# Kernel tuning notes

Hardware: AMD Instinct MI355X
Metric: run time of the kernel (lower is better)

## Reference

```python
import jax, jax.numpy as jnp
import numpy as np

N = 100_000          # ent_num
D = 256              # ent_dim
E_RAND = 3_200_000   # random edges (avg degree 32); + N self loops
NEG_SLOPE = 0.2      # LeakyReLU slope used by SpGraphAttentionLayer


def setup_inputs() -> dict:
    key = jax.random.key(0)
    k0, k1, k2, k3, k4, k5 = jax.random.split(key, 6)
    edges_rand = jax.random.randint(k0, (2, E_RAND), 0, N, dtype=jnp.int32)
    self_loops = jnp.tile(jnp.arange(N, dtype=jnp.int32)[None, :], (2, 1))
    edges = jnp.concatenate([edges_rand, self_loops], axis=1)  # [2, E]
    scale_w = 1.0 / np.sqrt(D).astype(np.float32)
    scale_a = 0.1 / np.sqrt(D).astype(np.float32)
    emb = jax.random.normal(k1, (N, D), jnp.float32)
    W1 = jax.random.normal(k2, (D, D), jnp.float32) * scale_w
    a1 = jax.random.normal(k3, (2 * D,), jnp.float32) * scale_a
    W2 = jax.random.normal(k4, (D, D), jnp.float32) * scale_w
    a2 = jax.random.normal(k5, (2 * D,), jnp.float32) * scale_a
    return {"emb": emb, "W1": W1, "a1": a1, "W2": W2, "a2": a2, "edges": edges}


def gat_layer(h, W, a, src, dst):
    # h: [N, D] node features; edges (src -> aggregates from dst)
    h2 = h @ W                              # [N, D]
    s_src = h2 @ a[:D]                      # [N] contribution of a . h_src
    s_dst = h2 @ a[D:]                      # [N] contribution of a . h_dst
    score = s_src[src] + s_dst[dst]         # [E] = a . [h_src; h_dst]
    e = jnp.exp(-jax.nn.leaky_relu(score, NEG_SLOPE))  # [E], pyGAT sparse form
    denom = jax.ops.segment_sum(e, src, num_segments=h.shape[0])          # [N]
    num = jax.ops.segment_sum(e[:, None] * h2[dst], src,
                              num_segments=h.shape[0])                    # [N, D]
    return jax.nn.elu(num / denom[:, None])


def reference(emb, W1, a1, W2, a2, edges):
    src, dst = edges[0], edges[1]
    h = gat_layer(emb, W1, a1, src, dst)
    h = gat_layer(h, W2, a2, src, dst)
    return h
```

## Files before the change

### kernel.cpp

```cpp
#include <hip/hip_runtime.h>
#include <hip/hip_bf16.h>

#define D 256
#define NEG_SLOPE 0.2f
#define BM 128
#define BN 128
#define BK 64
#define LDK 72

using bf16x8 = __attribute__((ext_vector_type(8))) __bf16;
using f32x4  = __attribute__((ext_vector_type(4))) float;
using u32x4  = __attribute__((ext_vector_type(4))) unsigned int;

__device__ __forceinline__ float bf2f(unsigned short u) {
    return __uint_as_float(((unsigned int)u) << 16);
}
__device__ __forceinline__ unsigned short f2bf(float f) {
    unsigned int u = __float_as_uint(f);
    unsigned int r = (u + 0x7FFF + ((u >> 16) & 1)) >> 16;
    return (unsigned short)r;
}


__global__ __launch_bounds__(256) void prep_kernel(
    const float* __restrict__ W1, const float* __restrict__ W2,
    unsigned short* __restrict__ WT1, unsigned short* __restrict__ WT2,
    int4* __restrict__ zbase, int nz16)
{
    const int b = blockIdx.x, tid = threadIdx.x;
    if (b < 256) {
        WT1[(size_t)tid * D + b] = f2bf(W1[(size_t)b * D + tid]);
    } else if (b < 512) {
        const int k = b - 256;
        WT2[(size_t)tid * D + k] = f2bf(W2[(size_t)k * D + tid]);
    } else {
        const int w = (b - 512) * 256 + tid;
        if (w < nz16) zbase[w] = make_int4(0, 0, 0, 0);
    }
}


__global__ void count_kernel(const int* __restrict__ src, int* __restrict__ counts, int E) {
    int t = blockIdx.x * blockDim.x + threadIdx.x;
    if (t < E) atomicAdd(&counts[src[t]], 1);
}

__global__ __launch_bounds__(1024) void scan_all_kernel(
    const int* __restrict__ counts, int* __restrict__ row_ptr, int n)
{
    __shared__ int ws[16];
    const int tid = threadIdx.x;
    const int lane = tid & 63, wv = tid >> 6;
    int base = 0;
    for (int c0 = 0; c0 < n; c0 += 4096) {
        const int idx = c0 + tid * 4;
        int4 v = make_int4(0, 0, 0, 0);
        if (idx + 3 < n) v = *(const int4*)(counts + idx);
        else {
            if (idx + 0 < n) v.x = counts[idx + 0];
            if (idx + 1 < n) v.y = counts[idx + 1];
            if (idx + 2 < n) v.z = counts[idx + 2];
            if (idx + 3 < n) v.w = counts[idx + 3];
        }
        const int s = v.x + v.y + v.z + v.w;
        int x = s;
        #pragma unroll
        for (int off = 1; off < 64; off <<= 1) {
            int t = __shfl_up(x, off);
            if (lane >= off) x += t;
        }
        if (lane == 63) ws[wv] = x;
        __syncthreads();
        int wo = base;
        #pragma unroll
        for (int w = 0; w < 16; ++w) if (w < wv) wo += ws[w];
        const int excl = wo + x - s;
        if (idx + 0 < n) row_ptr[idx + 0] = excl;
        if (idx + 1 < n) row_ptr[idx + 1] = excl + v.x;
        if (idx + 2 < n) row_ptr[idx + 2] = excl + v.x + v.y;
        if (idx + 3 < n) row_ptr[idx + 3] = excl + v.x + v.y + v.z;
        int tot = 0;
        #pragma unroll
        for (int w = 0; w < 16; ++w) tot += ws[w];
        __syncthreads();
        base += tot;
    }
    if (tid == 0) row_ptr[n] = base;
}

__global__ void fill_kernel(const int* __restrict__ src, const int* __restrict__ dst,
                            const int* __restrict__ row_ptr, int* __restrict__ fillp,
                            int* __restrict__ col, int E) {
    int t = blockIdx.x * blockDim.x + threadIdx.x;
    if (t < E) {
        int s = src[t];
        int pos = atomicAdd(&fillp[s], 1);
        col[row_ptr[s] + pos] = dst[t];
    }
}


__global__ __launch_bounds__(256) void gemm_mfma(
    const unsigned short* __restrict__ Ab, const float* __restrict__ Af,
    const unsigned short* __restrict__ BT,
    unsigned short* __restrict__ C, int M,
    const float* __restrict__ av, float* __restrict__ s_src, float* __restrict__ s_dst)
{
    __shared__ unsigned short smem[2 * BM * LDK];
    unsigned short* As_ = smem;
    unsigned short* Bs_ = smem + BM * LDK;
    const int tid = threadIdx.x;
    const int m0 = blockIdx.x * BM;
    const int n0 = blockIdx.y * BN;
    const int lane = tid & 63;
    const int wv = tid >> 6;
    const int wm = (wv & 1) * 64;
    const int wn = (wv >> 1) * 64;
    const int l15 = lane & 15;
    const int quad = lane >> 4;

    f32x4 acc[4][4];
    #pragma unroll
    for (int i = 0; i < 4; ++i)
        #pragma unroll
        for (int j = 0; j < 4; ++j)
            acc[i][j] = (f32x4){0.f, 0.f, 0.f, 0.f};

    for (int k0 = 0; k0 < D; k0 += BK) {
        #pragma unroll
        for (int c = tid; c < BM * 8; c += 256) {
            const int row = c >> 3, j = c & 7;
            const int gr = m0 + row;
            uint4 avv = make_uint4(0, 0, 0, 0);
            if (gr < M) {
                if (Af) {
                    const float* p = Af + (size_t)gr * D + k0 + j * 8;
                    const float4 f0 = *(const float4*)p;
                    const float4 f1 = *(const float4*)(p + 4);
                    avv.x = (unsigned int)f2bf(f0.x) | ((unsigned int)f2bf(f0.y) << 16);
                    avv.y = (unsigned int)f2bf(f0.z) | ((unsigned int)f2bf(f0.w) << 16);
                    avv.z = (unsigned int)f2bf(f1.x) | ((unsigned int)f2bf(f1.y) << 16);
                    avv.w = (unsigned int)f2bf(f1.z) | ((unsigned int)f2bf(f1.w) << 16);
                } else {
                    avv = *(const uint4*)(Ab + (size_t)gr * D + k0 + j * 8);
                }
            }
            *(uint4*)(As_ + row * LDK + j * 8) = avv;
            const uint4 bv = *(const uint4*)(BT + (size_t)(n0 + row) * D + k0 + j * 8);
            *(uint4*)(Bs_ + row * LDK + j * 8) = bv;
        }
        __syncthreads();
        #pragma unroll
        for (int s = 0; s < 2; ++s) {
            bf16x8 af[4], bfr[4];
            #pragma unroll
            for (int i = 0; i < 4; ++i)
                af[i] = *(const bf16x8*)(As_ + (wm + i * 16 + l15) * LDK + s * 32 + quad * 8);
            #pragma unroll
            for (int j = 0; j < 4; ++j)
                bfr[j] = *(const bf16x8*)(Bs_ + (wn + j * 16 + l15) * LDK + s * 32 + quad * 8);
            #pragma unroll
            for (int i = 0; i < 4; ++i)
                #pragma unroll
                for (int j = 0; j < 4; ++j)
                    acc[i][j] = __builtin_amdgcn_mfma_f32_16x16x32_bf16(
                        af[i], bfr[j], acc[i][j], 0, 0, 0);
        }
        __syncthreads();
    }

    unsigned short* Cw = smem + wv * (64 * LDK);
    #pragma unroll
    for (int i = 0; i < 4; ++i)
        #pragma unroll
        for (int j = 0; j < 4; ++j)
            #pragma unroll
            for (int r = 0; r < 4; ++r)
                Cw[(i * 16 + quad * 4 + r) * LDK + j * 16 + l15] = f2bf(acc[i][j][r]);
    __syncthreads();
    const int ccol = n0 + wn + (lane & 31) * 2;
    const float a1c0 = av[ccol],     a1c1 = av[ccol + 1];
    const float a2c0 = av[D + ccol], a2c1 = av[D + ccol + 1];
    #pragma unroll
    for (int rr = 0; rr < 64; rr += 2) {
        const int row = rr + (lane >> 5);
        const unsigned int wd = *(const unsigned int*)(Cw + row * LDK + (lane & 31) * 2);
        const int gr = m0 + wm + row;
        if (gr < M)
            *(unsigned int*)(C + (size_t)gr * D + ccol) = wd;
        const float f0 = bf2f((unsigned short)(wd & 0xffffu));
        const float f1 = bf2f((unsigned short)(wd >> 16));
        float p1 = f0 * a1c0 + f1 * a1c1;
        float p2 = f0 * a2c0 + f1 * a2c1;
        #pragma unroll
        for (int off = 16; off > 0; off >>= 1) {
            p1 += __shfl_xor(p1, off);
            p2 += __shfl_xor(p2, off);
        }
        if ((lane & 31) == 0 && gr < M) {
            atomicAdd(&s_src[gr], p1);
            atomicAdd(&s_dst[gr], p2);
        }
    }
}


__global__ __launch_bounds__(256) void agg_kernel(
    const unsigned short* __restrict__ h2, const float* __restrict__ s_src,
    const float* __restrict__ s_dst, const int* __restrict__ row_ptr,
    const int* __restrict__ col, unsigned short* __restrict__ out_bf16,
    float* __restrict__ out_f32, int Nn)
{
    const int lane = threadIdx.x & 63;
    const int half = lane >> 5;
    const int hl = lane & 31;
    const int node = blockIdx.x * 4 + (threadIdx.x >> 6);
    if (node >= Nn) return;
    const int beg = row_ptr[node], end = row_ptr[node + 1];
    const float ssrc = s_src[node];
    const unsigned short* hp = h2 + hl * 8;

    float a[8];
    #pragma unroll
    for (int i = 0; i < 8; ++i) a[i] = 0.f;
    float dpart = 0.f;

    for (int c0 = beg; c0 < end; c0 += 64) {
        const int cnt = min(64, end - c0);
        int j = 0;
        float e = 0.f;
        if (lane < cnt) {
            j = col[c0 + lane];
            const float sc = ssrc + s_dst[j];
            const float l = sc >= 0.f ? sc : NEG_SLOPE * sc;
            e = __expf(-l);
        }
        dpart += e;
        for (int k = 0; k < cnt; k += 8) {
            const int   j0 = __shfl(j, k + 0 + half);
            const int   j1 = __shfl(j, k + 2 + half);
            const int   j2 = __shfl(j, k + 4 + half);
            const int   j3 = __shfl(j, k + 6 + half);
            const float e0 = __shfl(e, k + 0 + half);
            const float e1 = __shfl(e, k + 2 + half);
            const float e2 = __shfl(e, k + 4 + half);
            const float e3 = __shfl(e, k + 6 + half);
            const uint4 u0 = *(const uint4*)(hp + (size_t)j0 * D);
            const uint4 u1 = *(const uint4*)(hp + (size_t)j1 * D);
            const uint4 u2 = *(const uint4*)(hp + (size_t)j2 * D);
            const uint4 u3 = *(const uint4*)(hp + (size_t)j3 * D);
            #define ACC8(u, ev)                                               \
                a[0] = fmaf(ev, __uint_as_float((u).x << 16), a[0]);          \
                a[1] = fmaf(ev, __uint_as_float((u).x & 0xffff0000u), a[1]);  \
                a[2] = fmaf(ev, __uint_as_float((u).y << 16), a[2]);          \
                a[3] = fmaf(ev, __uint_as_float((u).y & 0xffff0000u), a[3]);  \
                a[4] = fmaf(ev, __uint_as_float((u).z << 16), a[4]);          \
                a[5] = fmaf(ev, __uint_as_float((u).z & 0xffff0000u), a[5]);  \
                a[6] = fmaf(ev, __uint_as_float((u).w << 16), a[6]);          \
                a[7] = fmaf(ev, __uint_as_float((u).w & 0xffff0000u), a[7]);
            ACC8(u0, e0)
            ACC8(u1, e1)
            ACC8(u2, e2)
            ACC8(u3, e3)
            #undef ACC8
        }
    }

    #pragma unroll
    for (int i = 0; i < 8; ++i) a[i] += __shfl_xor(a[i], 32);

    float denom = dpart;
    #pragma unroll
    for (int off = 32; off > 0; off >>= 1) denom += __shfl_xor(denom, off);
    const float inv = 1.f / denom;

    if (half == 0) {
        float v[8];
        #pragma unroll
        for (int i = 0; i < 8; ++i) {
            const float x = a[i] * inv;
            v[i] = x > 0.f ? x : expm1f(x);
        }
        if (out_bf16) {
            u32x4 o;
            o.x = (unsigned int)f2bf(v[0]) | ((unsigned int)f2bf(v[1]) << 16);
            o.y = (unsigned int)f2bf(v[2]) | ((unsigned int)f2bf(v[3]) << 16);
            o.z = (unsigned int)f2bf(v[4]) | ((unsigned int)f2bf(v[5]) << 16);
            o.w = (unsigned int)f2bf(v[6]) | ((unsigned int)f2bf(v[7]) << 16);
            __builtin_nontemporal_store(o, (u32x4*)(out_bf16 + (size_t)node * D + hl * 8));
        } else {
            float* p = out_f32 + (size_t)node * D + hl * 8;
            f32x4 o0 = {v[0], v[1], v[2], v[3]};
            f32x4 o1 = {v[4], v[5], v[6], v[7]};
            __builtin_nontemporal_store(o0, (f32x4*)p);
            __builtin_nontemporal_store(o1, (f32x4*)(p + 4));
        }
    }
}


static inline size_t align_up(size_t x, size_t a) { return (x + a - 1) & ~(a - 1); }

extern "C" void kernel_launch(void* const* d_in, const int* in_sizes, int n_in,
                              void* d_out, int out_size, void* d_ws, size_t ws_size,
                              hipStream_t stream)
{
    const float* emb = (const float*)d_in[0];
    const float* W1  = (const float*)d_in[1];
    const float* a1  = (const float*)d_in[2];
    const float* W2  = (const float*)d_in[3];
    const float* a2  = (const float*)d_in[4];
    const int* edges = (const int*)d_in[5];
    const int Nn = in_sizes[0] / D;
    const int E  = in_sizes[5] / 2;
    const int* src = edges;
    const int* dst = edges + E;

    size_t off = 0;
    char* base = (char*)d_ws;
    unsigned short* hA = (unsigned short*)(base + off);
    off = align_up(off + (size_t)Nn * D * sizeof(unsigned short), 256);
    unsigned short* hB = (unsigned short*)(base + off);
    off = align_up(off + (size_t)Nn * D * sizeof(unsigned short), 256);
    unsigned short* WT1 = (unsigned short*)(base + off);
    off = align_up(off + (size_t)D * D * sizeof(unsigned short), 256);
    unsigned short* WT2 = (unsigned short*)(base + off);
    off = align_up(off + (size_t)D * D * sizeof(unsigned short), 256);

    const size_t cstride = align_up((size_t)Nn * sizeof(int), 256);
    char* zstart = base + off;
    float* s1s = (float*)(base + off); off += (size_t)Nn * sizeof(float);
    float* s1d = (float*)(base + off); off += (size_t)Nn * sizeof(float);
    float* s2s = (float*)(base + off); off += (size_t)Nn * sizeof(float);
    float* s2d = (float*)(base + off); off += (size_t)Nn * sizeof(float);
    off = align_up(off, 256);
    int* counts  = (int*)(base + off);   off += cstride;
    int* fillp   = (int*)(base + off);   off += cstride;
    const size_t zbytes = (size_t)(base + off - zstart);
    const int nz16 = (int)(zbytes / 16);

    int* row_ptr = (int*)(base + off);   off = align_up(off + (size_t)(Nn + 1) * sizeof(int), 256);
    int* col     = (int*)(base + off);   off = align_up(off + (size_t)E * sizeof(int), 256);

    const int zblocks = (nz16 + 255) / 256;
    prep_kernel<<<512 + zblocks, 256, 0, stream>>>(W1, W2, WT1, WT2, (int4*)zstart, nz16);

    count_kernel<<<(E + 255) / 256, 256, 0, stream>>>(src, counts, E);
    scan_all_kernel<<<1, 1024, 0, stream>>>(counts, row_ptr, Nn);
    fill_kernel<<<(E + 255) / 256, 256, 0, stream>>>(src, dst, row_ptr, fillp, col, E);

    dim3 ggrid((Nn + BM - 1) / BM, D / BN);
    gemm_mfma<<<ggrid, 256, 0, stream>>>(nullptr, emb, WT1, hA, Nn, a1, s1s, s1d);
    agg_kernel<<<(Nn + 3) / 4, 256, 0, stream>>>(hA, s1s, s1d, row_ptr, col, hB, nullptr, Nn);
    gemm_mfma<<<ggrid, 256, 0, stream>>>(hB, nullptr, WT2, hA, Nn, a2, s2s, s2d);
    agg_kernel<<<(Nn + 3) / 4, 256, 0, stream>>>(hA, s2s, s2d, row_ptr, col, nullptr,
                                                 (float*)d_out, Nn);
}
```

Measured before the change: 1.087 ms.

## Parallelize CSR prefix scan across blocks and use grid-stride count/fill/agg kernels

Replaces the single-block serial scan over all node counts with a three-phase scan: per-chunk sums, one small block scanning the chunk totals, then a parallel write of row offsets. The count, fill and aggregation kernels become grid-stride loops launched with a fixed 2048-block grid instead of one block per small work unit. The aim is to remove the long single-workgroup scan and reduce block launch overhead. It adds two extra small kernel launches, and the chunk scan assumes at most 128 chunks, so it only handles up to about 131K nodes.

```diff
diff --git a/kernel.cpp b/kernel.cpp
--- a/kernel.cpp
+++ b/kernel.cpp
@@ -7,6 +7,7 @@
 #define BN 128
 #define BK 64
 #define LDK 72
+#define SCAN_CHUNK 1024
 
 using bf16x8 = __attribute__((ext_vector_type(8))) __bf16;
 using f32x4  = __attribute__((ext_vector_type(4))) float;
@@ -41,58 +42,93 @@
 
 
 __global__ void count_kernel(const int* __restrict__ src, int* __restrict__ counts, int E) {
-    int t = blockIdx.x * blockDim.x + threadIdx.x;
-    if (t < E) atomicAdd(&counts[src[t]], 1);
-}
-
-__global__ __launch_bounds__(1024) void scan_all_kernel(
-    const int* __restrict__ counts, int* __restrict__ row_ptr, int n)
-{
-    __shared__ int ws[16];
+    const int stride = gridDim.x * blockDim.x;
+    for (int t = blockIdx.x * blockDim.x + threadIdx.x; t < E; t += stride)
+        atomicAdd(&counts[src[t]], 1);
+}
+
+__global__ __launch_bounds__(256) void scan_partial_kernel(
+    const int* __restrict__ counts, int* __restrict__ partial, int n)
+{
+    __shared__ int ws[4];
     const int tid = threadIdx.x;
     const int lane = tid & 63, wv = tid >> 6;
-    int base = 0;
-    for (int c0 = 0; c0 < n; c0 += 4096) {
-        const int idx = c0 + tid * 4;
-        int4 v = make_int4(0, 0, 0, 0);
-        if (idx + 3 < n) v = *(const int4*)(counts + idx);
-        else {
-            if (idx + 0 < n) v.x = counts[idx + 0];
-            if (idx + 1 < n) v.y = counts[idx + 1];
-            if (idx + 2 < n) v.z = counts[idx + 2];
-            if (idx + 3 < n) v.w = counts[idx + 3];
-        }
-        const int s = v.x + v.y + v.z + v.w;
-        int x = s;
-        #pragma unroll
-        for (int off = 1; off < 64; off <<= 1) {
-            int t = __shfl_up(x, off);
-            if (lane >= off) x += t;
-        }
-        if (lane == 63) ws[wv] = x;
+    const int idx = blockIdx.x * SCAN_CHUNK + tid * 4;
+    int4 v = make_int4(0, 0, 0, 0);
+    if (idx + 3 < n) v = *(const int4*)(counts + idx);
+    else {
+        if (idx + 0 < n) v.x = counts[idx + 0];
+        if (idx + 1 < n) v.y = counts[idx + 1];
+        if (idx + 2 < n) v.z = counts[idx + 2];
+        if (idx + 3 < n) v.w = counts[idx + 3];
+    }
+    int s = v.x + v.y + v.z + v.w;
+    #pragma unroll
+    for (int off = 32; off > 0; off >>= 1) s += __shfl_xor(s, off);
+    if (lane == 0) ws[wv] = s;
+    __syncthreads();
+    if (tid == 0) partial[blockIdx.x] = ws[0] + ws[1] + ws[2] + ws[3];
+}
+
+__global__ __launch_bounds__(128) void scan_chunks_kernel(
+    const int* __restrict__ partial, int* __restrict__ chunkoff,
+    int* __restrict__ row_ptr, int nchunks, int n)
+{
+    __shared__ int sm[128];
+    const int tid = threadIdx.x;
+    const int v = (tid < nchunks) ? partial[tid] : 0;
+    sm[tid] = v;
+    __syncthreads();
+    #pragma unroll
+    for (int off = 1; off < 128; off <<= 1) {
+        int t = (tid >= off) ? sm[tid - off] : 0;
         __syncthreads();
-        int wo = base;
-        #pragma unroll
-        for (int w = 0; w < 16; ++w) if (w < wv) wo += ws[w];
-        const int excl = wo + x - s;
-        if (idx + 0 < n) row_ptr[idx + 0] = excl;
-        if (idx + 1 < n) row_ptr[idx + 1] = excl + v.x;
-        if (idx + 2 < n) row_ptr[idx + 2] = excl + v.x + v.y;
-        if (idx + 3 < n) row_ptr[idx + 3] = excl + v.x + v.y + v.z;
-        int tot = 0;
-        #pragma unroll
-        for (int w = 0; w < 16; ++w) tot += ws[w];
+        sm[tid] += t;
         __syncthreads();
-        base += tot;
-    }
-    if (tid == 0) row_ptr[n] = base;
+    }
+    if (tid < nchunks) chunkoff[tid] = sm[tid] - v;
+    if (tid == 127) row_ptr[n] = sm[127];
+}
+
+__global__ __launch_bounds__(256) void scan_write_kernel(
+    const int* __restrict__ counts, const int* __restrict__ chunkoff,
+    int* __restrict__ row_ptr, int n)
+{
+    __shared__ int wsum[4];
+    const int tid = threadIdx.x;
+    const int lane = tid & 63, wv = tid >> 6;
+    const int idx = blockIdx.x * SCAN_CHUNK + tid * 4;
+    int4 v = make_int4(0, 0, 0, 0);
+    if (idx + 3 < n) v = *(const int4*)(counts + idx);
+    else {
+        if (idx + 0 < n) v.x = counts[idx + 0];
+        if (idx + 1 < n) v.y = counts[idx + 1];
+        if (idx + 2 < n) v.z = counts[idx + 2];
+        if (idx + 3 < n) v.w = counts[idx + 3];
+    }
+    const int s = v.x + v.y + v.z + v.w;
+    int x = s;
+    #pragma unroll
+    for (int off = 1; off < 64; off <<= 1) {
+        int t = __shfl_up(x, off);
+        if (lane >= off) x += t;
+    }
+    if (lane == 63) wsum[wv] = x;
+    __syncthreads();
+    int wo = chunkoff[blockIdx.x];
+    for (int w = 0; w < 4; ++w) if (w < wv) wo += wsum[w];
+    int excl = wo + x - s;
+    if (idx + 0 < n) row_ptr[idx + 0] = excl;
+    if (idx + 1 < n) row_ptr[idx + 1] = excl + v.x;
+    if (idx + 2 < n) row_ptr[idx + 2] = excl + v.x + v.y;
+    if (idx + 3 < n) row_ptr[idx + 3] = excl + v.x + v.y + v.z;
 }
 
 __global__ void fill_kernel(const int* __restrict__ src, const int* __restrict__ dst,
                             const int* __restrict__ row_ptr, int* __restrict__ fillp,
                             int* __restrict__ col, int E) {
-    int t = blockIdx.x * blockDim.x + threadIdx.x;
-    if (t < E) {
+    const int stride = gridDim.x * blockDim.x;
+    for (int t = blockIdx.x * blockDim.x + threadIdx.x; t < E; t += stride) {
         int s = src[t];
         int pos = atomicAdd(&fillp[s], 1);
         col[row_ptr[s] + pos] = dst[t];
@@ -214,86 +250,89 @@
     const int lane = threadIdx.x & 63;
     const int half = lane >> 5;
     const int hl = lane & 31;
-    const int node = blockIdx.x * 4 + (threadIdx.x >> 6);
-    if (node >= Nn) return;
-    const int beg = row_ptr[node], end = row_ptr[node + 1];
-    const float ssrc = s_src[node];
+    const int wid = blockIdx.x * 4 + (threadIdx.x >> 6);
+    const int nwaves = gridDim.x * 4;
     const unsigned short* hp = h2 + hl * 8;
 
-    float a[8];
-    #pragma unroll
-    for (int i = 0; i < 8; ++i) a[i] = 0.f;
-    float dpart = 0.f;
-
-    for (int c0 = beg; c0 < end; c0 += 64) {
-        const int cnt = min(64, end - c0);
-        int j = 0;
-        float e = 0.f;
-        if (lane < cnt) {
-            j = col[c0 + lane];
-            const float sc = ssrc + s_dst[j];
-            const float l = sc >= 0.f ? sc : NEG_SLOPE * sc;
-            e = __expf(-l);
-        }
-        dpart += e;
-        for (int k = 0; k < cnt; k += 8) {
-            const int   j0 = __shfl(j, k + 0 + half);
-            const int   j1 = __shfl(j, k + 2 + half);
-            const int   j2 = __shfl(j, k + 4 + half);
-            const int   j3 = __shfl(j, k + 6 + half);
-            const float e0 = __shfl(e, k + 0 + half);
-            const float e1 = __shfl(e, k + 2 + half);
-            const float e2 = __shfl(e, k + 4 + half);
-            const float e3 = __shfl(e, k + 6 + half);
-            const uint4 u0 = *(const uint4*)(hp + (size_t)j0 * D);
-            const uint4 u1 = *(const uint4*)(hp + (size_t)j1 * D);
-            const uint4 u2 = *(const uint4*)(hp + (size_t)j2 * D);
-            const uint4 u3 = *(const uint4*)(hp + (size_t)j3 * D);
-            #define ACC8(u, ev)                                               \
-                a[0] = fmaf(ev, __uint_as_float((u).x << 16), a[0]);          \
-                a[1] = fmaf(ev, __uint_as_float((u).x & 0xffff0000u), a[1]);  \
-                a[2] = fmaf(ev, __uint_as_float((u).y << 16), a[2]);          \
-                a[3] = fmaf(ev, __uint_as_float((u).y & 0xffff0000u), a[3]);  \
-                a[4] = fmaf(ev, __uint_as_float((u).z << 16), a[4]);          \
-                a[5] = fmaf(ev, __uint_as_float((u).z & 0xffff0000u), a[5]);  \
-                a[6] = fmaf(ev, __uint_as_float((u).w << 16), a[6]);          \
-                a[7] = fmaf(ev, __uint_as_float((u).w & 0xffff0000u), a[7]);
-            ACC8(u0, e0)
-            ACC8(u1, e1)
-            ACC8(u2, e2)
-            ACC8(u3, e3)
-            #undef ACC8
-        }
-    }
-
-    #pragma unroll
-    for (int i = 0; i < 8; ++i) a[i] += __shfl_xor(a[i], 32);
-
-    float denom = dpart;
-    #pragma unroll
-    for (int off = 32; off > 0; off >>= 1) denom += __shfl_xor(denom, off);
-    const float inv = 1.f / denom;
-
-    if (half == 0) {
-        float v[8];
-        #pragma unroll
-        for (int i = 0; i < 8; ++i) {
-            const float x = a[i] * inv;
-            v[i] = x > 0.f ? x : expm1f(x);
-        }
-        if (out_bf16) {
-            u32x4 o;
-            o.x = (unsigned int)f2bf(v[0]) | ((unsigned int)f2bf(v[1]) << 16);
-            o.y = (unsigned int)f2bf(v[2]) | ((unsigned int)f2bf(v[3]) << 16);
-            o.z = (unsigned int)f2bf(v[4]) | ((unsigned int)f2bf(v[5]) << 16);
-            o.w = (unsigned int)f2bf(v[6]) | ((unsigned int)f2bf(v[7]) << 16);
-            __builtin_nontemporal_store(o, (u32x4*)(out_bf16 + (size_t)node * D + hl * 8));
-        } else {
-            float* p = out_f32 + (size_t)node * D + hl * 8;
-            f32x4 o0 = {v[0], v[1], v[2], v[3]};
-            f32x4 o1 = {v[4], v[5], v[6], v[7]};
-            __builtin_nontemporal_store(o0, (f32x4*)p);
-            __builtin_nontemporal_store(o1, (f32x4*)(p + 4));
+    for (int node = wid; node < Nn; node += nwaves) {
+        const int beg = row_ptr[node], end = row_ptr[node + 1];
+        const float ssrc = s_src[node];
+
+        float a[8];
+        #pragma unroll
+        for (int i = 0; i < 8; ++i) a[i] = 0.f;
+        float dpart = 0.f;
+
+        for (int c0 = beg; c0 < end; c0 += 64) {
+            const int cnt = min(64, end - c0);
+            int j = 0;
+            float e = 0.f;
+            if (lane < cnt) {
+                j = col[c0 + lane];
+                const float sc = ssrc + s_dst[j];
+                const float l = sc >= 0.f ? sc : NEG_SLOPE * sc;
+                e = __expf(-l);
+            }
+            dpart += e;
+            for (int k = 0; k < cnt; k += 8) {
+                const int   j0 = __shfl(j, k + 0 + half);
+                const int   j1 = __shfl(j, k + 2 + half);
+                const int   j2 = __shfl(j, k + 4 + half);
+                const int   j3 = __shfl(j, k + 6 + half);
+                const float e0 = __shfl(e, k + 0 + half);
+                const float e1 = __shfl(e, k + 2 + half);
+                const float e2 = __shfl(e, k + 4 + half);
+                const float e3 = __shfl(e, k + 6 + half);
+                const uint4 u0 = *(const uint4*)(hp + (size_t)j0 * D);
+                const uint4 u1 = *(const uint4*)(hp + (size_t)j1 * D);
+                const uint4 u2 = *(const uint4*)(hp + (size_t)j2 * D);
+                const uint4 u3 = *(const uint4*)(hp + (size_t)j3 * D);
+                #define ACC8(u, ev)                                               \
+                    a[0] = fmaf(ev, __uint_as_float((u).x << 16), a[0]);          \
+                    a[1] = fmaf(ev, __uint_as_float((u).x & 0xffff0000u), a[1]);  \
+                    a[2] = fmaf(ev, __uint_as_float((u).y << 16), a[2]);          \
+                    a[3] = fmaf(ev, __uint_as_float((u).y & 0xffff0000u), a[3]);  \
+                    a[4] = fmaf(ev, __uint_as_float((u).z << 16), a[4]);          \
+                    a[5] = fmaf(ev, __uint_as_float((u).z & 0xffff0000u), a[5]);  \
+                    a[6] = fmaf(ev, __uint_as_float((u).w << 16), a[6]);          \
+                    a[7] = fmaf(ev, __uint_as_float((u).w & 0xffff0000u), a[7]);
+                ACC8(u0, e0)
+                ACC8(u1, e1)
+                ACC8(u2, e2)
+                ACC8(u3, e3)
+                #undef ACC8
+            }
+        }
+
+        #pragma unroll
+        for (int i = 0; i < 8; ++i) a[i] += __shfl_xor(a[i], 32);
+
+        float denom = dpart;
+        #pragma unroll
+        for (int off = 32; off > 0; off >>= 1) denom += __shfl_xor(denom, off);
+        const float inv = 1.f / denom;
+
+        if (half == 0) {
+            float v[8];
+            #pragma unroll
+            for (int i = 0; i < 8; ++i) {
+                const float x = a[i] * inv;
+                v[i] = x > 0.f ? x : expm1f(x);
+            }
+            if (out_bf16) {
+                u32x4 o;
+                o.x = (unsigned int)f2bf(v[0]) | ((unsigned int)f2bf(v[1]) << 16);
+                o.y = (unsigned int)f2bf(v[2]) | ((unsigned int)f2bf(v[3]) << 16);
+                o.z = (unsigned int)f2bf(v[4]) | ((unsigned int)f2bf(v[5]) << 16);
+                o.w = (unsigned int)f2bf(v[6]) | ((unsigned int)f2bf(v[7]) << 16);
+                __builtin_nontemporal_store(o, (u32x4*)(out_bf16 + (size_t)node * D + hl * 8));
+            } else {
+                float* p = out_f32 + (size_t)node * D + hl * 8;
+                f32x4 o0 = {v[0], v[1], v[2], v[3]};
+                f32x4 o1 = {v[4], v[5], v[6], v[7]};
+                __builtin_nontemporal_store(o0, (f32x4*)p);
+                __builtin_nontemporal_store(o1, (f32x4*)(p + 4));
+            }
         }
     }
 }
@@ -315,6 +354,7 @@
     const int E  = in_sizes[5] / 2;
     const int* src = edges;
     const int* dst = edges + E;
+    const int nchunks = (Nn + SCAN_CHUNK - 1) / SCAN_CHUNK;
 
     size_t off = 0;
     char* base = (char*)d_ws;
@@ -340,19 +380,23 @@
     const int nz16 = (int)(zbytes / 16);
 
     int* row_ptr = (int*)(base + off);   off = align_up(off + (size_t)(Nn + 1) * sizeof(int), 256);
+    int* partial = (int*)(base + off);   off = align_up(off + (size_t)nchunks * sizeof(int), 256);
+    int* chunkoff= (int*)(base + off);   off = align_up(off + (size_t)nchunks * sizeof(int), 256);
     int* col     = (int*)(base + off);   off = align_up(off + (size_t)E * sizeof(int), 256);
 
     const int zblocks = (nz16 + 255) / 256;
     prep_kernel<<<512 + zblocks, 256, 0, stream>>>(W1, W2, WT1, WT2, (int4*)zstart, nz16);
 
-    count_kernel<<<(E + 255) / 256, 256, 0, stream>>>(src, counts, E);
-    scan_all_kernel<<<1, 1024, 0, stream>>>(counts, row_ptr, Nn);
-    fill_kernel<<<(E + 255) / 256, 256, 0, stream>>>(src, dst, row_ptr, fillp, col, E);
+    count_kernel<<<2048, 256, 0, stream>>>(src, counts, E);
+    scan_partial_kernel<<<nchunks, 256, 0, stream>>>(counts, partial, Nn);
+    scan_chunks_kernel<<<1, 128, 0, stream>>>(partial, chunkoff, row_ptr, nchunks, Nn);
+    scan_write_kernel<<<nchunks, 256, 0, stream>>>(counts, chunkoff, row_ptr, Nn);
+    fill_kernel<<<2048, 256, 0, stream>>>(src, dst, row_ptr, fillp, col, E);
 
     dim3 ggrid((Nn + BM - 1) / BM, D / BN);
     gemm_mfma<<<ggrid, 256, 0, stream>>>(nullptr, emb, WT1, hA, Nn, a1, s1s, s1d);
-    agg_kernel<<<(Nn + 3) / 4, 256, 0, stream>>>(hA, s1s, s1d, row_ptr, col, hB, nullptr, Nn);
+    agg_kernel<<<2048, 256, 0, stream>>>(hA, s1s, s1d, row_ptr, col, hB, nullptr, Nn);
     gemm_mfma<<<ggrid, 256, 0, stream>>>(hB, nullptr, WT2, hA, Nn, a2, s2s, s2d);
-    agg_kernel<<<(Nn + 3) / 4, 256, 0, stream>>>(hA, s2s, s2d, row_ptr, col, nullptr,
-                                                 (float*)d_out, Nn);
-}
+    agg_kernel<<<2048, 256, 0, stream>>>(hA, s2s, s2d, row_ptr, col, nullptr,
+                                         (float*)d_out, Nn);
+}
```

After: 1.089 ms. No clear change (+0.2%).
